# Kernel optimization log

Hardware: AMD Instinct MI355X
Metric: run time of the kernel (lower is better)

## Reference

```python
import jax, jax.numpy as jnp
import numpy as np


def _lstm_scan(x_proj, Wr, units):
    """x_proj: [T, B, 4U] precomputed x@Wk + b. Keras gate order: i, f, g(c), o.
    Returns (all_h [T,B,U], last_h [B,U])."""
    B = x_proj.shape[1]
    h0 = jnp.zeros((B, units), x_proj.dtype)
    c0 = jnp.zeros((B, units), x_proj.dtype)

    def step(carry, xt):
        h, c = carry
        z = xt + h @ Wr                      # [B, 4U]
        i, f, g, o = jnp.split(z, 4, axis=-1)
        i = jax.nn.sigmoid(i)
        f = jax.nn.sigmoid(f)
        g = jnp.tanh(g)
        o = jax.nn.sigmoid(o)
        c = f * c + i * g
        h = o * jnp.tanh(c)
        return (h, c), h

    (h_T, _), hs = jax.lax.scan(step, (h0, c0), x_proj)
    return hs, h_T


def bilstm(x, Wk_f, Wr_f, b_f, Wk_b, Wr_b, b_b):
    units = Wr_f.shape[0]
    # Precompute input projections for all timesteps (one big GEMM per direction)
    xp_f = (x @ Wk_f + b_f).transpose(1, 0, 2)             # [T, B, 4U]
    xp_b = (x[:, ::-1] @ Wk_b + b_b).transpose(1, 0, 2)    # reversed time

    fw_hs, fw_last = _lstm_scan(xp_f, Wr_f, units)         # [T,B,U], [B,U]
    bw_hs, bw_last = _lstm_scan(xp_b, Wr_b, units)

    fw_outputs = fw_hs.transpose(1, 0, 2)                  # [B, T, U]
    # go_backwards outputs are in reverse time order; K.reverse(_, 1) re-aligns
    bw_outputs = bw_hs.transpose(1, 0, 2)[:, ::-1]         # [B, T, U]

    outputs = jnp.concatenate([fw_outputs, bw_outputs], axis=-1)   # [B, T, 2U]
    last_output = jnp.concatenate([fw_last, bw_last], axis=-1)     # [B, 2U]
    return outputs, last_output


def setup_inputs() -> dict:
    key = jax.random.key(0)
    ks = jax.random.split(key, 6)
    B, T, D, U = 32, 512, 256, 256
    s_in = 1.0 / np.sqrt(D)
    s_rec = 1.0 / np.sqrt(U)
    return {
        "x": jax.random.normal(ks[0], (B, T, D), jnp.float32),
        "Wk_f": jax.random.normal(ks[1], (D, 4 * U), jnp.float32) * s_in,
        "Wr_f": jax.random.normal(ks[2], (U, 4 * U), jnp.float32) * s_rec,
        "b_f": jnp.zeros((4 * U,), jnp.float32),
        "Wk_b": jax.random.normal(ks[3], (D, 4 * U), jnp.float32) * s_in,
        "Wr_b": jax.random.normal(ks[4], (U, 4 * U), jnp.float32) * s_rec,
        "b_b": jnp.zeros((4 * U,), jnp.float32),
    }


def reference(x, Wk_f, Wr_f, b_f, Wk_b, Wr_b, b_b):
    return bilstm(x, Wk_f, Wr_f, b_f, Wk_b, Wr_b, b_b)
```

## Files before the change

### kernel.cpp

```cpp
#include <hip/hip_runtime.h>

#define T_STEPS 512
#define BATCH   32
#define DIM     256
#define UNITS   256
#define COLS4U  1024

typedef _Float16 half8  __attribute__((ext_vector_type(8)));
typedef _Float16 half4v __attribute__((ext_vector_type(4)));
typedef float    f32x4  __attribute__((ext_vector_type(4)));
typedef unsigned long long ull;
typedef ull      ull2   __attribute__((ext_vector_type(2)));

__device__ __forceinline__ float fsig(float x){ return 1.0f/(1.0f+__expf(-x)); }
__device__ __forceinline__ float ftanh(float x){
  float xx = fminf(fmaxf(x,-15.f),15.f);
  float e = __expf(2.f*xx);
  return (e-1.f)/(e+1.f);
}

__device__ __forceinline__ int swz(int b, int u){
  int g = u >> 3;
  int s = (g & 7) ^ (b & 7);
  return b*512 + (g>>3)*128 + s*16 + (u & 7)*2;
}

__global__ __launch_bounds__(256, 2) void xproj(
    const float* __restrict__ x,
    const float* __restrict__ Wk_f, const float* __restrict__ b_f,
    const float* __restrict__ Wk_b, const float* __restrict__ b_b,
    _Float16* __restrict__ xph)
{
  const int bx  = blockIdx.x;
  const int dir = bx >> 8;
  const int cg  = (bx >> 5) & 7;
  const int tg  = bx & 31;
  const int tid = threadIdx.x;
  const int w   = tid >> 6;
  const int lane= tid & 63;
  const int l15 = lane & 15;
  const int l4  = lane >> 4;

  const float* Wk = dir ? Wk_b : Wk_f;
  const float* bs = dir ? b_b  : b_f;

  const int col0 = cg*128 + w*32;

  half8 Bf[2][8];
  float bias[2];
#pragma unroll
  for (int nt=0; nt<2; nt++){
    const int col = col0 + nt*16 + l15;
    bias[nt] = bs[col];
#pragma unroll
    for (int kk=0; kk<8; kk++){
      half8 v;
#pragma unroll
      for (int r=0; r<8; r++) v[r] = (_Float16)Wk[(size_t)(kk*32 + l4*8 + r)*COLS4U + col];
      Bf[nt][kk] = v;
    }
  }

  for (int tt=0; tt<16; ++tt){
    const int t   = tg*16 + tt;
    const int tin = dir ? (T_STEPS-1-t) : t;

    half8 Af[2][8];
#pragma unroll
    for (int mt=0; mt<2; mt++){
      const int b = mt*16 + l15;
#pragma unroll
      for (int kk=0; kk<8; kk++){
        const float* xp_ = x + ((size_t)b*T_STEPS + tin)*DIM + kk*32 + l4*8;
        f32x4 u0 = *(const f32x4*)xp_;
        f32x4 u1 = *(const f32x4*)(xp_ + 4);
        half8 v;
        v[0]=(_Float16)u0[0]; v[1]=(_Float16)u0[1]; v[2]=(_Float16)u0[2]; v[3]=(_Float16)u0[3];
        v[4]=(_Float16)u1[0]; v[5]=(_Float16)u1[1]; v[6]=(_Float16)u1[2]; v[7]=(_Float16)u1[3];
        Af[mt][kk] = v;
      }
    }

    f32x4 acc[2][2];
#pragma unroll
    for (int nt=0; nt<2; nt++){
      f32x4 a; a[0]=bias[nt]; a[1]=bias[nt]; a[2]=bias[nt]; a[3]=bias[nt];
      acc[nt][0]=a; acc[nt][1]=a;
    }
#pragma unroll
    for (int kk=0; kk<8; kk++)
#pragma unroll
      for (int nt=0; nt<2; nt++)
#pragma unroll
        for (int mt=0; mt<2; mt++)
          acc[nt][mt] = __builtin_amdgcn_mfma_f32_16x16x32_f16(Af[mt][kk], Bf[nt][kk], acc[nt][mt], 0,0,0);

#pragma unroll
    for (int nt=0; nt<2; nt++){
      const int col = col0 + nt*16 + l15;
#pragma unroll
      for (int mt=0; mt<2; mt++){
        half4v o;
        o[0]=(_Float16)acc[nt][mt][0]; o[1]=(_Float16)acc[nt][mt][1];
        o[2]=(_Float16)acc[nt][mt][2]; o[3]=(_Float16)acc[nt][mt][3];
        *(ull*)(xph + ((size_t)(dir*T_STEPS + t)*COLS4U + col)*BATCH + mt*16 + l4*4)
            = __builtin_bit_cast(ull, o);
      }
    }
  }
}

__global__ __launch_bounds__(512, 2) void bilstm_scan4(
    const float* __restrict__ Wr_f, const float* __restrict__ Wr_b,
    float* __restrict__ out,
    const _Float16* __restrict__ xph,
    unsigned* __restrict__ slices)
{
  const int dir  = blockIdx.x >> 1;
  const int half = blockIdx.x & 1;
  const int tid  = threadIdx.x;
  const int w    = tid >> 6;
  const int lane = tid & 63;
  const int l15  = lane & 15;
  const int l4   = lane >> 4;

  const float* Wr = dir ? Wr_b : Wr_f;

  const int uloc   = w*16 + l15;
  const int unit   = half*128 + uloc;
  const int outcol = dir*256 + unit;

  __shared__ _Float16 hlds[2][BATCH*UNITS];

  half8 Bf[4][8];
#pragma unroll
  for (int q=0; q<4; q++){
    const int col = q*256 + unit;
#pragma unroll
    for (int kk=0; kk<8; kk++){
      half8 v;
#pragma unroll
      for (int r=0; r<8; r++) v[r] = (_Float16)Wr[(size_t)(kk*32 + l4*8 + r)*COLS4U + col];
      Bf[q][kk] = v;
      __builtin_amdgcn_sched_barrier(0);
    }
  }

  {
    half8 z;
#pragma unroll
    for (int e=0; e<8; e++) z[e] = (_Float16)0.f;
    for (int i=tid; i<BATCH*UNITS/8; i+=512) ((half8*)hlds[0])[i] = z;
  }
  __syncthreads();

  const int b_r = tid >> 4;
  const int c0  = (tid & 15) * 8;
  const int pbase = (1-half)*128;

  float cst[8];
#pragma unroll
  for (int i=0;i<8;i++) cst[i]=0.f;
  bool spin_ok = true;

  ull xpv[8];
#pragma unroll
  for (int q=0;q<4;q++)
#pragma unroll
    for (int mt=0;mt<2;mt++)
      xpv[q*2+mt] = *(const ull*)(xph + ((size_t)(dir*T_STEPS + 0)*COLS4U + q*256+unit)*BATCH + mt*16 + l4*4);

  for (int t=0; t<T_STEPS; ++t){
    f32x4 acc[2][4];
#pragma unroll
    for (int q=0;q<4;q++)
#pragma unroll
      for (int mt=0;mt<2;mt++){
        half4v hv = __builtin_bit_cast(half4v, xpv[q*2+mt]);
        f32x4 a; a[0]=(float)hv[0]; a[1]=(float)hv[1]; a[2]=(float)hv[2]; a[3]=(float)hv[3];
        acc[mt][q] = a;
      }

    const char* hpl = (const char*)hlds[t&1];
#pragma unroll
    for (int kk=0; kk<8; kk++){
      const int ul = kk*32 + l4*8;
      half8 a0 = *(const half8*)(hpl + swz(l15,    ul));
      half8 a1 = *(const half8*)(hpl + swz(16+l15, ul));
#pragma unroll
      for (int q=0;q<4;q++){
        acc[0][q] = __builtin_amdgcn_mfma_f32_16x16x32_f16(a0, Bf[q][kk], acc[0][q], 0,0,0);
        acc[1][q] = __builtin_amdgcn_mfma_f32_16x16x32_f16(a1, Bf[q][kk], acc[1][q], 0,0,0);
      }
    }

    const int tout = dir ? (T_STEPS-1-t) : t;
    const int par  = (t+1) & 1;
    unsigned* myslc = slices + ((size_t)(par*4 + dir*2 + half))*4096;
    const unsigned tgt_out = (unsigned)(t+1) & 0xFFFFu;
    char* hnx = (char*)hlds[(t+1)&1];
#pragma unroll
    for (int mt=0; mt<2; mt++){
#pragma unroll
      for (int r=0;r<4;r++){
        const int b = mt*16 + l4*4 + r;
        float iv = fsig (acc[mt][0][r]);
        float fv = fsig (acc[mt][1][r]);
        float gv = ftanh(acc[mt][2][r]);
        float ov = fsig (acc[mt][3][r]);
        float &c = cst[mt*4+r];
        c = fv*c + iv*gv;
        float hv = ov*ftanh(c);
        _Float16 hf = (_Float16)hv;
        if (t+1 < T_STEPS){
          unsigned word = ((unsigned)__builtin_bit_cast(unsigned short, hf) << 16) | tgt_out;
          __hip_atomic_store(&myslc[b*128 + uloc], word,
                             __ATOMIC_RELAXED, __HIP_MEMORY_SCOPE_AGENT);
        }
        *(_Float16*)(hnx + swz(b, unit)) = hf;
        out[((size_t)b*T_STEPS + tout)*(2*UNITS) + outcol] = hv;
        if (t == T_STEPS-1)
          out[(size_t)BATCH*T_STEPS*(2*UNITS) + (size_t)b*(2*UNITS) + outcol] = hv;
      }
    }

    if (t+1 < T_STEPS){
#pragma unroll
      for (int q=0;q<4;q++)
#pragma unroll
        for (int mt=0;mt<2;mt++)
          xpv[q*2+mt] = *(const ull*)(xph + ((size_t)(dir*T_STEPS + (t+1))*COLS4U + q*256+unit)*BATCH + mt*16 + l4*4);

      const ull* src = (const ull*)(slices + ((size_t)(par*4 + dir*2 + (1-half)))*4096
                                    + b_r*128 + c0);
      ull v0,v1,v2,v3;
      if (spin_ok){
        int sp = 0; bool ok;
        do {
          v0 = __hip_atomic_load(&src[0], __ATOMIC_RELAXED, __HIP_MEMORY_SCOPE_AGENT);
          v1 = __hip_atomic_load(&src[1], __ATOMIC_RELAXED, __HIP_MEMORY_SCOPE_AGENT);
          v2 = __hip_atomic_load(&src[2], __ATOMIC_RELAXED, __HIP_MEMORY_SCOPE_AGENT);
          v3 = __hip_atomic_load(&src[3], __ATOMIC_RELAXED, __HIP_MEMORY_SCOPE_AGENT);
          unsigned t0=(unsigned)v0, t1=(unsigned)(v0>>32), t2=(unsigned)v1, t3=(unsigned)(v1>>32);
          unsigned t4=(unsigned)v2, t5=(unsigned)(v2>>32), t6=(unsigned)v3, t7=(unsigned)(v3>>32);
          ok = ((t0&0xFFFF)==tgt_out) & ((t1&0xFFFF)==tgt_out) & ((t2&0xFFFF)==tgt_out)
             & ((t3&0xFFFF)==tgt_out) & ((t4&0xFFFF)==tgt_out) & ((t5&0xFFFF)==tgt_out)
             & ((t6&0xFFFF)==tgt_out) & ((t7&0xFFFF)==tgt_out);
          if (++sp > (1<<20)) { spin_ok = false; break; }
        } while(!ok);
      } else {
        v0 = __hip_atomic_load(&src[0], __ATOMIC_RELAXED, __HIP_MEMORY_SCOPE_AGENT);
        v1 = __hip_atomic_load(&src[1], __ATOMIC_RELAXED, __HIP_MEMORY_SCOPE_AGENT);
        v2 = __hip_atomic_load(&src[2], __ATOMIC_RELAXED, __HIP_MEMORY_SCOPE_AGENT);
        v3 = __hip_atomic_load(&src[3], __ATOMIC_RELAXED, __HIP_MEMORY_SCOPE_AGENT);
      }
      half8 hv;
      {
        unsigned wlo, whi;
        wlo=(unsigned)v0; whi=(unsigned)(v0>>32);
        hv[0]=__builtin_bit_cast(_Float16,(unsigned short)(wlo>>16));
        hv[1]=__builtin_bit_cast(_Float16,(unsigned short)(whi>>16));
        wlo=(unsigned)v1; whi=(unsigned)(v1>>32);
        hv[2]=__builtin_bit_cast(_Float16,(unsigned short)(wlo>>16));
        hv[3]=__builtin_bit_cast(_Float16,(unsigned short)(whi>>16));
        wlo=(unsigned)v2; whi=(unsigned)(v2>>32);
        hv[4]=__builtin_bit_cast(_Float16,(unsigned short)(wlo>>16));
        hv[5]=__builtin_bit_cast(_Float16,(unsigned short)(whi>>16));
        wlo=(unsigned)v3; whi=(unsigned)(v3>>32);
        hv[6]=__builtin_bit_cast(_Float16,(unsigned short)(wlo>>16));
        hv[7]=__builtin_bit_cast(_Float16,(unsigned short)(whi>>16));
      }
      *(half8*)(hnx + swz(b_r, pbase + c0)) = hv;
    }
    __syncthreads();
  }
}

__global__ __launch_bounds__(256,1) void bilstm_mfma(
    const float* __restrict__ x,
    const float* __restrict__ Wk_f, const float* __restrict__ Wr_f, const float* __restrict__ b_f,
    const float* __restrict__ Wk_b, const float* __restrict__ Wr_b, const float* __restrict__ b_b,
    float* __restrict__ out,
    unsigned short* __restrict__ slices,
    unsigned* __restrict__ flags)
{
  const int dir = blockIdx.x >> 2;
  const int g4  = blockIdx.x & 3;
  const int tid = threadIdx.x;
  const int w   = tid >> 6;
  const int lane= tid & 63;
  const int l15 = lane & 15;
  const int l4  = lane >> 4;

  const float* Wk = dir ? Wk_b : Wk_f;
  const float* Wr = dir ? Wr_b : Wr_f;
  const float* bs = dir ? b_b  : b_f;

  const int u0b   = g4*64;
  const int upl   = u0b + w*16 + l15;
  const int outcol= dir*256 + upl;

  __shared__ _Float16 xlds[BATCH*DIM];
  __shared__ _Float16 hlds[2][BATCH*UNITS];

  half8 Bf[4][16];
#pragma unroll
  for (int q=0;q<4;q++){
    const int col = q*256 + upl;
#pragma unroll
    for (int kk=0;kk<16;kk++){
      const float* Ws = (kk<8) ? Wk : Wr;
      const int k0 = (kk&7)*32 + l4*8;
      half8 v;
#pragma unroll
      for (int r=0;r<8;r++) v[r] = (_Float16)Ws[(size_t)(k0+r)*COLS4U + col];
      Bf[q][kk] = v;
      __builtin_amdgcn_sched_barrier(0);
    }
  }

  float bias[4];
#pragma unroll
  for (int q=0;q<4;q++) bias[q] = bs[q*256 + upl];

  {
    half8 z;
#pragma unroll
    for (int e=0;e<8;e++) z[e] = (_Float16)0.f;
    for (int i=tid; i<BATCH*UNITS/8; i+=256) ((half8*)hlds[0])[i] = z;
  }

  const int bx  = tid >> 3;
  const int d0x = (tid & 7) * 32;
  float xr[32];
  {
    const int tin0 = dir ? (T_STEPS-1) : 0;
    const float* xp = x + ((size_t)bx*T_STEPS + tin0)*DIM + d0x;
#pragma unroll
    for (int i=0;i<8;i++){
      f32x4 v = *(const f32x4*)(xp + i*4);
      xr[i*4+0]=v[0]; xr[i*4+1]=v[1]; xr[i*4+2]=v[2]; xr[i*4+3]=v[3];
    }
#pragma unroll
    for (int j=0;j<4;j++){
      half8 hh;
#pragma unroll
      for (int e=0;e<8;e++) hh[e] = (_Float16)xr[j*8+e];
      *(half8*)((char*)xlds + swz(bx, d0x + j*8)) = hh;
    }
  }
  __syncthreads();

  float cst[8];
#pragma unroll
  for (int i=0;i<8;i++) cst[i]=0.f;
  bool spin_ok = true;

  for (int t=0; t<T_STEPS; ++t){
    if (t+1 < T_STEPS){
      const int tin = dir ? (T_STEPS-2-t) : (t+1);
      const float* xp = x + ((size_t)bx*T_STEPS + tin)*DIM + d0x;
#pragma unroll
      for (int i=0;i<8;i++){
        f32x4 v = *(const f32x4*)(xp + i*4);
        xr[i*4+0]=v[0]; xr[i*4+1]=v[1]; xr[i*4+2]=v[2]; xr[i*4+3]=v[3];
      }
    }

    f32x4 acc[2][4];
#pragma unroll
    for (int q=0;q<4;q++){
      f32x4 a; a[0]=bias[q]; a[1]=bias[q]; a[2]=bias[q]; a[3]=bias[q];
      acc[0][q]=a; acc[1][q]=a;
    }
    const char* hpl = (const char*)hlds[t&1];
#pragma unroll
    for (int kk=0;kk<16;kk++){
      const char* pl = (kk<8) ? (const char*)xlds : hpl;
      const int ul = (kk&7)*32 + l4*8;
      half8 a0 = *(const half8*)(pl + swz(l15,      ul));
      half8 a1 = *(const half8*)(pl + swz(16+l15,   ul));
#pragma unroll
      for (int q=0;q<4;q++){
        acc[0][q] = __builtin_amdgcn_mfma_f32_16x16x32_f16(a0, Bf[q][kk], acc[0][q], 0,0,0);
        acc[1][q] = __builtin_amdgcn_mfma_f32_16x16x32_f16(a1, Bf[q][kk], acc[1][q], 0,0,0);
      }
    }

    const int tout = dir ? (T_STEPS-1-t) : t;
    unsigned short* slc = slices + (((size_t)((t+1)&1))*8 + dir*4 + g4)*2048;
    char* hnx = (char*)hlds[(t+1)&1];
#pragma unroll
    for (int mt=0; mt<2; mt++){
#pragma unroll
      for (int r=0;r<4;r++){
        const int b = mt*16 + l4*4 + r;
        float iv = fsig (acc[mt][0][r]);
        float fv = fsig (acc[mt][1][r]);
        float gv = ftanh(acc[mt][2][r]);
        float ov = fsig (acc[mt][3][r]);
        float &c = cst[mt*4+r];
        c = fv*c + iv*gv;
        float hval = ov*ftanh(c);
        out[((size_t)b*T_STEPS + tout)*(2*UNITS) + outcol] = hval;
        if (t == T_STEPS-1)
          out[(size_t)BATCH*T_STEPS*(2*UNITS) + (size_t)b*(2*UNITS) + outcol] = hval;
        _Float16 hf = (_Float16)hval;
        *(_Float16*)(hnx + swz(b, upl)) = hf;
        if (t+1 < T_STEPS)
          __hip_atomic_store(&slc[b*64 + (w*16+l15)],
                             __builtin_bit_cast(unsigned short, hf),
                             __ATOMIC_RELAXED, __HIP_MEMORY_SCOPE_AGENT);
      }
    }
    __syncthreads();

    if (t+1 < T_STEPS){
      if (tid == 192)
        __hip_atomic_store(&flags[(dir*4+g4)*32], (unsigned)(t+1),
                           __ATOMIC_RELAXED, __HIP_MEMORY_SCOPE_AGENT);
#pragma unroll
      for (int j=0;j<4;j++){
        half8 hh;
#pragma unroll
        for (int e=0;e<8;e++) hh[e] = (_Float16)xr[j*8+e];
        *(half8*)((char*)xlds + swz(bx, d0x + j*8)) = hh;
      }
      if (w < 3){
        const int p = w + (w >= g4);
        const unsigned target = (unsigned)(t+1);
        if (spin_ok){
          int sp = 0;
          while (__hip_atomic_load(&flags[(dir*4+p)*32],
                                   __ATOMIC_RELAXED, __HIP_MEMORY_SCOPE_AGENT) < target){
            if (++sp > (1<<22)) { spin_ok = false; break; }
          }
        }
        const ull* src = (const ull*)(slices + (((size_t)((t+1)&1))*8 + dir*4 + p)*2048);
        const int bsl = lane >> 1;
        const int u00 = (lane & 1) * 32;
#pragma unroll
        for (int j=0;j<4;j++){
          ull v0 = __hip_atomic_load(&src[lane*8 + 2*j  ], __ATOMIC_RELAXED, __HIP_MEMORY_SCOPE_AGENT);
          ull v1 = __hip_atomic_load(&src[lane*8 + 2*j+1], __ATOMIC_RELAXED, __HIP_MEMORY_SCOPE_AGENT);
          ull2 vv; vv[0]=v0; vv[1]=v1;
          *(ull2*)(hnx + swz(bsl, p*64 + u00 + j*8)) = vv;
        }
      }
      __syncthreads();
    }
  }
}

extern "C" void kernel_launch(void* const* d_in, const int* in_sizes, int n_in,
                              void* d_out, int out_size, void* d_ws, size_t ws_size,
                              hipStream_t stream) {
  const float* x    = (const float*)d_in[0];
  const float* Wk_f = (const float*)d_in[1];
  const float* Wr_f = (const float*)d_in[2];
  const float* b_f  = (const float*)d_in[3];
  const float* Wk_b = (const float*)d_in[4];
  const float* Wr_b = (const float*)d_in[5];
  const float* b_b  = (const float*)d_in[6];
  float* out = (float*)d_out;

  const size_t XPH = (size_t)2*T_STEPS*COLS4U*BATCH*sizeof(_Float16);
  const size_t SL  = (size_t)2*2*2*BATCH*128*sizeof(unsigned);

  if (ws_size >= XPH + SL) {
    _Float16* xph    = (_Float16*)d_ws;
    unsigned* slices = (unsigned*)((char*)d_ws + XPH);
    xproj<<<512, 256, 0, stream>>>(x, Wk_f, b_f, Wk_b, b_b, xph);
    bilstm_scan4<<<4, 512, 0, stream>>>(Wr_f, Wr_b, out, xph, slices);
  } else {
    unsigned short* slices = (unsigned short*)d_ws;
    unsigned* flags = (unsigned*)((char*)d_ws + 65536);
    hipMemsetAsync((char*)d_ws + 65536, 0, 1024, stream);
    bilstm_mfma<<<8, 256, 0, stream>>>(x, Wk_f, Wr_f, b_f, Wk_b, Wr_b, b_b,
                                       out, slices, flags);
  }
}
```

Measured before the change: 2.842 ms.

## Split LSTM scan across 8 blocks placed on shared XCDs via runtime election

Replaces the 4-block (2 per direction, 512 threads) recurrent scan with 8 blocks of 256 threads, 4 per direction, each owning 64 units. The kernel launches 64 candidate blocks, which record their XCC_ID in a registration table and then elect blocks that share an XCD. When placement succeeds, h exchange uses volatile stores and loads instead of agent-scope atomics, on the expectation that same-XCD L2 coherence makes plain accesses visible. This halves per-block MFMA work per step but requires every step to gather slices from three peers instead of one, and its correctness rests on the co-location assumption and on spin timeouts.

Result: slower. 6.429 ms (+126.2%).

```diff
diff --git a/kernel.cpp b/kernel.cpp
--- a/kernel.cpp
+++ b/kernel.cpp
@@ -5,6 +5,7 @@
 #define DIM     256
 #define UNITS   256
 #define COLS4U  1024
+#define NCAND   64
 
 typedef _Float16 half8  __attribute__((ext_vector_type(8)));
 typedef _Float16 half4v __attribute__((ext_vector_type(4)));
@@ -14,15 +15,13 @@
 
 __device__ __forceinline__ float fsig(float x){ return 1.0f/(1.0f+__expf(-x)); }
 __device__ __forceinline__ float ftanh(float x){
-  float xx = fminf(fmaxf(x,-15.f),15.f);
-  float e = __expf(2.f*xx);
+  float xx=fminf(fmaxf(x,-15.f),15.f);
+  float e=__expf(2.f*xx);
   return (e-1.f)/(e+1.f);
 }
-
-__device__ __forceinline__ int swz(int b, int u){
-  int g = u >> 3;
-  int s = (g & 7) ^ (b & 7);
-  return b*512 + (g>>3)*128 + s*16 + (u & 7)*2;
+__device__ __forceinline__ int swz(int b,int u){
+  int g=u>>3; int s=(g&7)^(b&7);
+  return b*512 + (g>>3)*128 + s*16 + (u&7)*2;
 }
 
 __global__ __launch_bounds__(256, 2) void xproj(
@@ -110,38 +109,26 @@
   }
 }
 
-__global__ __launch_bounds__(512, 2) void bilstm_scan4(
-    const float* __restrict__ Wr_f, const float* __restrict__ Wr_b,
-    float* __restrict__ out,
-    const _Float16* __restrict__ xph,
-    unsigned* __restrict__ slices)
+template<int MODE>
+__device__ __forceinline__ void scan_body(
+    int dir, int g4, const float* __restrict__ Wr, float* __restrict__ out,
+    const _Float16* __restrict__ xph, unsigned* __restrict__ slices,
+    _Float16 (*hlds)[BATCH*UNITS])
 {
-  const int dir  = blockIdx.x >> 1;
-  const int half = blockIdx.x & 1;
-  const int tid  = threadIdx.x;
-  const int w    = tid >> 6;
-  const int lane = tid & 63;
-  const int l15  = lane & 15;
-  const int l4   = lane >> 4;
-
-  const float* Wr = dir ? Wr_b : Wr_f;
-
-  const int uloc   = w*16 + l15;
-  const int unit   = half*128 + uloc;
-  const int outcol = dir*256 + unit;
-
-  __shared__ _Float16 hlds[2][BATCH*UNITS];
+  const int tid=threadIdx.x;
+  const int w=tid>>6, lane=tid&63, l15=lane&15, l4=lane>>4;
+  const int uloc=w*16+l15, unit=g4*64+uloc, outcol=dir*256+unit;
 
   half8 Bf[4][8];
 #pragma unroll
-  for (int q=0; q<4; q++){
-    const int col = q*256 + unit;
-#pragma unroll
-    for (int kk=0; kk<8; kk++){
+  for(int q=0;q<4;q++){
+    const int col=q*256+unit;
+#pragma unroll
+    for(int kk=0;kk<8;kk++){
       half8 v;
 #pragma unroll
-      for (int r=0; r<8; r++) v[r] = (_Float16)Wr[(size_t)(kk*32 + l4*8 + r)*COLS4U + col];
-      Bf[q][kk] = v;
+      for(int r=0;r<8;r++) v[r]=(_Float16)Wr[(size_t)(kk*32+l4*8+r)*COLS4U+col];
+      Bf[q][kk]=v;
       __builtin_amdgcn_sched_barrier(0);
     }
   }
@@ -149,131 +136,176 @@
   {
     half8 z;
 #pragma unroll
-    for (int e=0; e<8; e++) z[e] = (_Float16)0.f;
-    for (int i=tid; i<BATCH*UNITS/8; i+=512) ((half8*)hlds[0])[i] = z;
+    for(int e=0;e<8;e++) z[e]=(_Float16)0.f;
+    for(int i=tid;i<BATCH*UNITS/8;i+=256) ((half8*)hlds[0])[i]=z;
   }
   __syncthreads();
 
-  const int b_r = tid >> 4;
-  const int c0  = (tid & 15) * 8;
-  const int pbase = (1-half)*128;
-
   float cst[8];
 #pragma unroll
-  for (int i=0;i<8;i++) cst[i]=0.f;
-  bool spin_ok = true;
+  for(int i=0;i<8;i++) cst[i]=0.f;
+  bool spin_ok=true;
 
   ull xpv[8];
 #pragma unroll
-  for (int q=0;q<4;q++)
-#pragma unroll
-    for (int mt=0;mt<2;mt++)
-      xpv[q*2+mt] = *(const ull*)(xph + ((size_t)(dir*T_STEPS + 0)*COLS4U + q*256+unit)*BATCH + mt*16 + l4*4);
-
-  for (int t=0; t<T_STEPS; ++t){
+  for(int q=0;q<4;q++)
+#pragma unroll
+    for(int mt=0;mt<2;mt++)
+      xpv[q*2+mt]=*(const ull*)(xph+((size_t)(dir*T_STEPS+0)*COLS4U+q*256+unit)*BATCH+mt*16+l4*4);
+
+  const int b_r=lane>>1, u0r=(lane&1)*32;
+  const int pw=(w<3)?(w+(w>=g4)):0;
+
+  for(int t=0;t<T_STEPS;++t){
     f32x4 acc[2][4];
 #pragma unroll
-    for (int q=0;q<4;q++)
-#pragma unroll
-      for (int mt=0;mt<2;mt++){
-        half4v hv = __builtin_bit_cast(half4v, xpv[q*2+mt]);
-        f32x4 a; a[0]=(float)hv[0]; a[1]=(float)hv[1]; a[2]=(float)hv[2]; a[3]=(float)hv[3];
-        acc[mt][q] = a;
-      }
-
-    const char* hpl = (const char*)hlds[t&1];
-#pragma unroll
-    for (int kk=0; kk<8; kk++){
-      const int ul = kk*32 + l4*8;
-      half8 a0 = *(const half8*)(hpl + swz(l15,    ul));
-      half8 a1 = *(const half8*)(hpl + swz(16+l15, ul));
-#pragma unroll
-      for (int q=0;q<4;q++){
-        acc[0][q] = __builtin_amdgcn_mfma_f32_16x16x32_f16(a0, Bf[q][kk], acc[0][q], 0,0,0);
-        acc[1][q] = __builtin_amdgcn_mfma_f32_16x16x32_f16(a1, Bf[q][kk], acc[1][q], 0,0,0);
-      }
-    }
-
-    const int tout = dir ? (T_STEPS-1-t) : t;
-    const int par  = (t+1) & 1;
-    unsigned* myslc = slices + ((size_t)(par*4 + dir*2 + half))*4096;
-    const unsigned tgt_out = (unsigned)(t+1) & 0xFFFFu;
-    char* hnx = (char*)hlds[(t+1)&1];
-#pragma unroll
-    for (int mt=0; mt<2; mt++){
-#pragma unroll
-      for (int r=0;r<4;r++){
-        const int b = mt*16 + l4*4 + r;
-        float iv = fsig (acc[mt][0][r]);
-        float fv = fsig (acc[mt][1][r]);
-        float gv = ftanh(acc[mt][2][r]);
-        float ov = fsig (acc[mt][3][r]);
-        float &c = cst[mt*4+r];
-        c = fv*c + iv*gv;
-        float hv = ov*ftanh(c);
-        _Float16 hf = (_Float16)hv;
-        if (t+1 < T_STEPS){
-          unsigned word = ((unsigned)__builtin_bit_cast(unsigned short, hf) << 16) | tgt_out;
-          __hip_atomic_store(&myslc[b*128 + uloc], word,
-                             __ATOMIC_RELAXED, __HIP_MEMORY_SCOPE_AGENT);
+    for(int q=0;q<4;q++)
+#pragma unroll
+      for(int mt=0;mt<2;mt++){
+        half4v hv=__builtin_bit_cast(half4v,xpv[q*2+mt]);
+        f32x4 a; a[0]=(float)hv[0];a[1]=(float)hv[1];a[2]=(float)hv[2];a[3]=(float)hv[3];
+        acc[mt][q]=a;
+      }
+
+    const char* hpl=(const char*)hlds[t&1];
+#pragma unroll
+    for(int kk=0;kk<8;kk++){
+      const int ul=kk*32+l4*8;
+      half8 a0=*(const half8*)(hpl+swz(l15,ul));
+      half8 a1=*(const half8*)(hpl+swz(16+l15,ul));
+#pragma unroll
+      for(int q=0;q<4;q++){
+        acc[0][q]=__builtin_amdgcn_mfma_f32_16x16x32_f16(a0,Bf[q][kk],acc[0][q],0,0,0);
+        acc[1][q]=__builtin_amdgcn_mfma_f32_16x16x32_f16(a1,Bf[q][kk],acc[1][q],0,0,0);
+      }
+    }
+
+    const int tout=dir?(T_STEPS-1-t):t;
+    const int par=(t+1)&1;
+    unsigned* myslc=slices+((size_t)(par*8+dir*4+g4))*2048;
+    const unsigned tgt=(unsigned)(t+1)&0xFFFFu;
+    char* hnx=(char*)hlds[(t+1)&1];
+#pragma unroll
+    for(int mt=0;mt<2;mt++){
+#pragma unroll
+      for(int r=0;r<4;r++){
+        const int b=mt*16+l4*4+r;
+        float iv=fsig(acc[mt][0][r]);
+        float fv=fsig(acc[mt][1][r]);
+        float gv=ftanh(acc[mt][2][r]);
+        float ov=fsig(acc[mt][3][r]);
+        float &c=cst[mt*4+r];
+        c=fv*c+iv*gv;
+        float hv=ov*ftanh(c);
+        _Float16 hf=(_Float16)hv;
+        if(t+1<T_STEPS){
+          unsigned word=((unsigned)__builtin_bit_cast(unsigned short,hf)<<16)|tgt;
+          if(MODE==0) *(volatile unsigned*)&myslc[b*64+uloc]=word;
+          else __hip_atomic_store(&myslc[b*64+uloc],word,__ATOMIC_RELAXED,__HIP_MEMORY_SCOPE_AGENT);
         }
-        *(_Float16*)(hnx + swz(b, unit)) = hf;
-        out[((size_t)b*T_STEPS + tout)*(2*UNITS) + outcol] = hv;
-        if (t == T_STEPS-1)
-          out[(size_t)BATCH*T_STEPS*(2*UNITS) + (size_t)b*(2*UNITS) + outcol] = hv;
-      }
-    }
-
-    if (t+1 < T_STEPS){
-#pragma unroll
-      for (int q=0;q<4;q++)
-#pragma unroll
-        for (int mt=0;mt<2;mt++)
-          xpv[q*2+mt] = *(const ull*)(xph + ((size_t)(dir*T_STEPS + (t+1))*COLS4U + q*256+unit)*BATCH + mt*16 + l4*4);
-
-      const ull* src = (const ull*)(slices + ((size_t)(par*4 + dir*2 + (1-half)))*4096
-                                    + b_r*128 + c0);
-      ull v0,v1,v2,v3;
-      if (spin_ok){
-        int sp = 0; bool ok;
-        do {
-          v0 = __hip_atomic_load(&src[0], __ATOMIC_RELAXED, __HIP_MEMORY_SCOPE_AGENT);
-          v1 = __hip_atomic_load(&src[1], __ATOMIC_RELAXED, __HIP_MEMORY_SCOPE_AGENT);
-          v2 = __hip_atomic_load(&src[2], __ATOMIC_RELAXED, __HIP_MEMORY_SCOPE_AGENT);
-          v3 = __hip_atomic_load(&src[3], __ATOMIC_RELAXED, __HIP_MEMORY_SCOPE_AGENT);
-          unsigned t0=(unsigned)v0, t1=(unsigned)(v0>>32), t2=(unsigned)v1, t3=(unsigned)(v1>>32);
-          unsigned t4=(unsigned)v2, t5=(unsigned)(v2>>32), t6=(unsigned)v3, t7=(unsigned)(v3>>32);
-          ok = ((t0&0xFFFF)==tgt_out) & ((t1&0xFFFF)==tgt_out) & ((t2&0xFFFF)==tgt_out)
-             & ((t3&0xFFFF)==tgt_out) & ((t4&0xFFFF)==tgt_out) & ((t5&0xFFFF)==tgt_out)
-             & ((t6&0xFFFF)==tgt_out) & ((t7&0xFFFF)==tgt_out);
-          if (++sp > (1<<20)) { spin_ok = false; break; }
-        } while(!ok);
-      } else {
-        v0 = __hip_atomic_load(&src[0], __ATOMIC_RELAXED, __HIP_MEMORY_SCOPE_AGENT);
-        v1 = __hip_atomic_load(&src[1], __ATOMIC_RELAXED, __HIP_MEMORY_SCOPE_AGENT);
-        v2 = __hip_atomic_load(&src[2], __ATOMIC_RELAXED, __HIP_MEMORY_SCOPE_AGENT);
-        v3 = __hip_atomic_load(&src[3], __ATOMIC_RELAXED, __HIP_MEMORY_SCOPE_AGENT);
-      }
-      half8 hv;
-      {
-        unsigned wlo, whi;
-        wlo=(unsigned)v0; whi=(unsigned)(v0>>32);
-        hv[0]=__builtin_bit_cast(_Float16,(unsigned short)(wlo>>16));
-        hv[1]=__builtin_bit_cast(_Float16,(unsigned short)(whi>>16));
-        wlo=(unsigned)v1; whi=(unsigned)(v1>>32);
-        hv[2]=__builtin_bit_cast(_Float16,(unsigned short)(wlo>>16));
-        hv[3]=__builtin_bit_cast(_Float16,(unsigned short)(whi>>16));
-        wlo=(unsigned)v2; whi=(unsigned)(v2>>32);
-        hv[4]=__builtin_bit_cast(_Float16,(unsigned short)(wlo>>16));
-        hv[5]=__builtin_bit_cast(_Float16,(unsigned short)(whi>>16));
-        wlo=(unsigned)v3; whi=(unsigned)(v3>>32);
-        hv[6]=__builtin_bit_cast(_Float16,(unsigned short)(wlo>>16));
-        hv[7]=__builtin_bit_cast(_Float16,(unsigned short)(whi>>16));
-      }
-      *(half8*)(hnx + swz(b_r, pbase + c0)) = hv;
+        *(_Float16*)(hnx+swz(b,unit))=hf;
+        out[((size_t)b*T_STEPS+tout)*(2*UNITS)+outcol]=hv;
+        if(t==T_STEPS-1)
+          out[(size_t)BATCH*T_STEPS*(2*UNITS)+(size_t)b*(2*UNITS)+outcol]=hv;
+      }
+    }
+
+    if(t+1<T_STEPS){
+#pragma unroll
+      for(int q=0;q<4;q++)
+#pragma unroll
+        for(int mt=0;mt<2;mt++)
+          xpv[q*2+mt]=*(const ull*)(xph+((size_t)(dir*T_STEPS+(t+1))*COLS4U+q*256+unit)*BATCH+mt*16+l4*4);
+
+      if(w<3){
+        const unsigned* src=slices+((size_t)(par*8+dir*4+pw))*2048 + b_r*64 + u0r;
+        unsigned wbuf[32];
+        if(spin_ok){
+          int sp=0; bool ok;
+          do{
+            ok=true;
+#pragma unroll
+            for(int k=0;k<32;k++){
+              unsigned v=(MODE==0)? *(volatile const unsigned*)(src+k)
+                 : __hip_atomic_load(src+k,__ATOMIC_RELAXED,__HIP_MEMORY_SCOPE_AGENT);
+              wbuf[k]=v; ok &= ((v&0xFFFFu)==tgt);
+            }
+            if(++sp>(1<<17)){spin_ok=false;break;}
+          }while(!ok);
+        } else {
+#pragma unroll
+          for(int k=0;k<32;k++)
+            wbuf[k]=(MODE==0)? *(volatile const unsigned*)(src+k)
+               : __hip_atomic_load(src+k,__ATOMIC_RELAXED,__HIP_MEMORY_SCOPE_AGENT);
+        }
+#pragma unroll
+        for(int j=0;j<4;j++){
+          half8 hh;
+#pragma unroll
+          for(int e=0;e<8;e++)
+            hh[e]=__builtin_bit_cast(_Float16,(unsigned short)(wbuf[j*8+e]>>16));
+          *(half8*)(hnx+swz(b_r,pw*64+u0r+j*8))=hh;
+        }
+      }
     }
     __syncthreads();
   }
+}
+
+__global__ __launch_bounds__(256,1) void bilstm_scan_xcd(
+    const float* __restrict__ Wr_f, const float* __restrict__ Wr_b,
+    float* __restrict__ out, const _Float16* __restrict__ xph,
+    unsigned* __restrict__ slices, unsigned* __restrict__ regtab)
+{
+  __shared__ _Float16 hlds[2][BATCH*UNITS];
+  __shared__ unsigned stab[NCAND];
+  __shared__ int sinfo[2];
+  const int tid=threadIdx.x;
+
+  if(tid==0){
+    unsigned xv;
+    asm volatile("s_getreg_b32 %0, hwreg(HW_REG_XCC_ID)":"=s"(xv));
+    __hip_atomic_store(&regtab[blockIdx.x],0x100u|(xv&0xFu),
+                       __ATOMIC_RELAXED,__HIP_MEMORY_SCOPE_AGENT);
+  }
+  if(tid<NCAND){
+    unsigned v; int sp=0;
+    for(;;){
+      v=__hip_atomic_load(&regtab[tid],__ATOMIC_RELAXED,__HIP_MEMORY_SCOPE_AGENT);
+      if(__all((v&0x100u)!=0)) break;
+      if(++sp>(1<<17)) break;
+    }
+    stab[tid]=v;
+  }
+  __syncthreads();
+
+  if(tid==0){
+    bool full=true;
+    for(int i=0;i<NCAND;i++) if(!(stab[i]&0x100u)){full=false;break;}
+    int role=-1, mode=0;
+    if(full){
+      int cnt[8]={0,0,0,0,0,0,0,0};
+      for(int i=0;i<NCAND;i++) cnt[stab[i]&7]++;
+      int x0=-1,x1=-1;
+      for(int a=0;a<8;a++) if(cnt[a]>=4){x0=a;break;}
+      for(int a=0;a<8;a++) if(a!=x0&&cnt[a]>=4){x1=a;break;}
+      if(x1<0) x1=x0;
+      const int myb=(int)blockIdx.x;
+      const int myx=stab[myb]&7;
+      int rank=0;
+      for(int i=0;i<myb;i++) if((stab[i]&7)==myx) rank++;
+      if(x1==x0){ if(myx==x0&&rank<8) role=rank; }
+      else{ if(myx==x0&&rank<4) role=rank; else if(myx==x1&&rank<4) role=4+rank; }
+    } else { mode=1; if(blockIdx.x<8) role=(int)blockIdx.x; }
+    sinfo[0]=role; sinfo[1]=mode;
+  }
+  __syncthreads();
+  const int role=sinfo[0];
+  if(role<0) return;
+  const int dir=role>>2, g4=role&3;
+  const float* Wr=dir?Wr_b:Wr_f;
+  if(sinfo[1]==0) scan_body<0>(dir,g4,Wr,out,xph,slices,hlds);
+  else            scan_body<1>(dir,g4,Wr,out,xph,slices,hlds);
 }
 
 __global__ __launch_bounds__(256,1) void bilstm_mfma(
@@ -465,13 +497,16 @@
   float* out = (float*)d_out;
 
   const size_t XPH = (size_t)2*T_STEPS*COLS4U*BATCH*sizeof(_Float16);
-  const size_t SL  = (size_t)2*2*2*BATCH*128*sizeof(unsigned);
-
-  if (ws_size >= XPH + SL) {
+  const size_t SL  = (size_t)2*8*2048*sizeof(unsigned);
+  const size_t RT  = 256;
+
+  if (ws_size >= XPH + SL + RT) {
     _Float16* xph    = (_Float16*)d_ws;
     unsigned* slices = (unsigned*)((char*)d_ws + XPH);
+    unsigned* regtab = (unsigned*)((char*)d_ws + XPH + SL);
+    hipMemsetAsync(regtab, 0, RT, stream);
     xproj<<<512, 256, 0, stream>>>(x, Wk_f, b_f, Wk_b, b_b, xph);
-    bilstm_scan4<<<4, 512, 0, stream>>>(Wr_f, Wr_b, out, xph, slices);
+    bilstm_scan_xcd<<<NCAND, 256, 0, stream>>>(Wr_f, Wr_b, out, xph, slices, regtab);
   } else {
     unsigned short* slices = (unsigned short*)d_ws;
     unsigned* flags = (unsigned*)((char*)d_ws + 65536);
```

## Co-locate scan blocks on one XCC and exchange hidden state via L2-coherent loads

Applied to the files above, without the earlier changes.

The scan kernel now launches 64 candidate blocks that each report their XCC id. Block 0 then picks four blocks sharing an XCC to run the four direction/half roles, and the remaining blocks exit. The hidden-state exchange between the two halves uses sc0 global loads and stores (intended to stay coherent within one XCC's L2), with a fallback to the agent-scope atomic path after a spin timeout. This aims to cut cross-XCC communication latency per timestep, at the cost of an extra memset, a registration handshake, dual stores, and reliance on all candidate blocks being co-resident.

Measured after the change: 9.428 ms. +231.7%, slower.

```diff
diff --git a/kernel.cpp b/kernel.cpp
--- a/kernel.cpp
+++ b/kernel.cpp
@@ -5,24 +5,35 @@
 #define DIM     256
 #define UNITS   256
 #define COLS4U  1024
+#define NCAND   64
 
 typedef _Float16 half8  __attribute__((ext_vector_type(8)));
 typedef _Float16 half4v __attribute__((ext_vector_type(4)));
 typedef float    f32x4  __attribute__((ext_vector_type(4)));
+typedef unsigned uint4v __attribute__((ext_vector_type(4)));
 typedef unsigned long long ull;
 typedef ull      ull2   __attribute__((ext_vector_type(2)));
 
 __device__ __forceinline__ float fsig(float x){ return 1.0f/(1.0f+__expf(-x)); }
 __device__ __forceinline__ float ftanh(float x){
-  float xx = fminf(fmaxf(x,-15.f),15.f);
-  float e = __expf(2.f*xx);
+  float xx=fminf(fmaxf(x,-15.f),15.f);
+  float e=__expf(2.f*xx);
   return (e-1.f)/(e+1.f);
 }
-
-__device__ __forceinline__ int swz(int b, int u){
-  int g = u >> 3;
-  int s = (g & 7) ^ (b & 7);
-  return b*512 + (g>>3)*128 + s*16 + (u & 7)*2;
+__device__ __forceinline__ int swz(int b,int u){
+  int g=u>>3; int s=(g&7)^(b&7);
+  return b*512 + (g>>3)*128 + s*16 + (u&7)*2;
+}
+
+__device__ __forceinline__ void ld8_sc0(const unsigned* p, uint4v& a, uint4v& b){
+  asm volatile(
+    "global_load_dwordx4 %0, %2, off sc0\n\t"
+    "global_load_dwordx4 %1, %2, off offset:16 sc0\n\t"
+    "s_waitcnt vmcnt(0)"
+    : "=&v"(a), "=&v"(b) : "v"(p) : "memory");
+}
+__device__ __forceinline__ void st1_sc0(unsigned* p, unsigned v){
+  asm volatile("global_store_dword %0, %1, off sc0" :: "v"(p), "v"(v) : "memory");
 }
 
 __global__ __launch_bounds__(256, 2) void xproj(
@@ -110,27 +121,22 @@
   }
 }
 
-__global__ __launch_bounds__(512, 2) void bilstm_scan4(
-    const float* __restrict__ Wr_f, const float* __restrict__ Wr_b,
-    float* __restrict__ out,
+__device__ __forceinline__ void scan_body(
+    int dir, int half_, bool fast0,
+    const float* __restrict__ Wr, float* __restrict__ out,
     const _Float16* __restrict__ xph,
-    unsigned* __restrict__ slices)
+    unsigned* __restrict__ fastslc, unsigned* __restrict__ safeslc,
+    _Float16 (*hlds)[BATCH*UNITS])
 {
-  const int dir  = blockIdx.x >> 1;
-  const int half = blockIdx.x & 1;
   const int tid  = threadIdx.x;
   const int w    = tid >> 6;
   const int lane = tid & 63;
   const int l15  = lane & 15;
   const int l4   = lane >> 4;
 
-  const float* Wr = dir ? Wr_b : Wr_f;
-
   const int uloc   = w*16 + l15;
-  const int unit   = half*128 + uloc;
+  const int unit   = half_*128 + uloc;
   const int outcol = dir*256 + unit;
-
-  __shared__ _Float16 hlds[2][BATCH*UNITS];
 
   half8 Bf[4][8];
 #pragma unroll
@@ -156,12 +162,13 @@
 
   const int b_r = tid >> 4;
   const int c0  = (tid & 15) * 8;
-  const int pbase = (1-half)*128;
+  const int pbase = (1-half_)*128;
 
   float cst[8];
 #pragma unroll
   for (int i=0;i<8;i++) cst[i]=0.f;
-  bool spin_ok = true;
+  bool use_fast = fast0;
+  bool safe_ok  = true;
 
   ull xpv[8];
 #pragma unroll
@@ -196,8 +203,8 @@
 
     const int tout = dir ? (T_STEPS-1-t) : t;
     const int par  = (t+1) & 1;
-    unsigned* myslc = slices + ((size_t)(par*4 + dir*2 + half))*4096;
-    const unsigned tgt_out = (unsigned)(t+1) & 0xFFFFu;
+    const size_t wslot = ((size_t)(par*4 + dir*2 + half_))*4096;
+    const unsigned tgt = (unsigned)(t+1) & 0xFFFFu;
     char* hnx = (char*)hlds[(t+1)&1];
 #pragma unroll
     for (int mt=0; mt<2; mt++){
@@ -213,8 +220,9 @@
         float hv = ov*ftanh(c);
         _Float16 hf = (_Float16)hv;
         if (t+1 < T_STEPS){
-          unsigned word = ((unsigned)__builtin_bit_cast(unsigned short, hf) << 16) | tgt_out;
-          __hip_atomic_store(&myslc[b*128 + uloc], word,
+          unsigned word = ((unsigned)__builtin_bit_cast(unsigned short, hf) << 16) | tgt;
+          st1_sc0(&fastslc[wslot + b*128 + uloc], word);
+          __hip_atomic_store(&safeslc[wslot + b*128 + uloc], word,
                              __ATOMIC_RELAXED, __HIP_MEMORY_SCOPE_AGENT);
         }
         *(_Float16*)(hnx + swz(b, unit)) = hf;
@@ -231,49 +239,127 @@
         for (int mt=0;mt<2;mt++)
           xpv[q*2+mt] = *(const ull*)(xph + ((size_t)(dir*T_STEPS + (t+1))*COLS4U + q*256+unit)*BATCH + mt*16 + l4*4);
 
-      const ull* src = (const ull*)(slices + ((size_t)(par*4 + dir*2 + (1-half)))*4096
-                                    + b_r*128 + c0);
-      ull v0,v1,v2,v3;
-      if (spin_ok){
-        int sp = 0; bool ok;
-        do {
-          v0 = __hip_atomic_load(&src[0], __ATOMIC_RELAXED, __HIP_MEMORY_SCOPE_AGENT);
-          v1 = __hip_atomic_load(&src[1], __ATOMIC_RELAXED, __HIP_MEMORY_SCOPE_AGENT);
-          v2 = __hip_atomic_load(&src[2], __ATOMIC_RELAXED, __HIP_MEMORY_SCOPE_AGENT);
-          v3 = __hip_atomic_load(&src[3], __ATOMIC_RELAXED, __HIP_MEMORY_SCOPE_AGENT);
-          unsigned t0=(unsigned)v0, t1=(unsigned)(v0>>32), t2=(unsigned)v1, t3=(unsigned)(v1>>32);
-          unsigned t4=(unsigned)v2, t5=(unsigned)(v2>>32), t6=(unsigned)v3, t7=(unsigned)(v3>>32);
-          ok = ((t0&0xFFFF)==tgt_out) & ((t1&0xFFFF)==tgt_out) & ((t2&0xFFFF)==tgt_out)
-             & ((t3&0xFFFF)==tgt_out) & ((t4&0xFFFF)==tgt_out) & ((t5&0xFFFF)==tgt_out)
-             & ((t6&0xFFFF)==tgt_out) & ((t7&0xFFFF)==tgt_out);
-          if (++sp > (1<<20)) { spin_ok = false; break; }
-        } while(!ok);
+      const size_t rslot = ((size_t)(par*4 + dir*2 + (1-half_)))*4096;
+      const unsigned* fsrc = fastslc + rslot + b_r*128 + c0;
+      const unsigned* ssrc = safeslc + rslot + b_r*128 + c0;
+      unsigned wv[8];
+      bool got = false;
+
+      if (use_fast){
+        int sp = 0;
+        for(;;){
+          uint4v a, b2;
+          ld8_sc0(fsrc, a, b2);
+          wv[0]=a[0]; wv[1]=a[1]; wv[2]=a[2]; wv[3]=a[3];
+          wv[4]=b2[0]; wv[5]=b2[1]; wv[6]=b2[2]; wv[7]=b2[3];
+          bool ok = true;
+#pragma unroll
+          for (int k=0;k<8;k++) ok &= ((wv[k]&0xFFFFu)==tgt);
+          if (ok){ got = true; break; }
+          if (++sp > 4096){ use_fast = false; break; }
+        }
+      }
+      if (!got){
+        if (safe_ok){
+          int sp = 0;
+          for(;;){
+            bool ok = true;
+#pragma unroll
+            for (int k=0;k<8;k++){
+              wv[k] = __hip_atomic_load(ssrc+k, __ATOMIC_RELAXED, __HIP_MEMORY_SCOPE_AGENT);
+              ok &= ((wv[k]&0xFFFFu)==tgt);
+            }
+            if (ok) break;
+            if (++sp > (1<<20)){ safe_ok = false; break; }
+          }
+        } else {
+#pragma unroll
+          for (int k=0;k<8;k++)
+            wv[k] = __hip_atomic_load(ssrc+k, __ATOMIC_RELAXED, __HIP_MEMORY_SCOPE_AGENT);
+        }
+      }
+
+      half8 hh;
+#pragma unroll
+      for (int e=0;e<8;e++)
+        hh[e] = __builtin_bit_cast(_Float16,(unsigned short)(wv[e]>>16));
+      *(half8*)(hnx + swz(b_r, pbase + c0)) = hh;
+    }
+    __syncthreads();
+  }
+}
+
+__global__ __launch_bounds__(512,1) void bilstm_scan_pair(
+    const float* __restrict__ Wr_f, const float* __restrict__ Wr_b,
+    float* __restrict__ out, const _Float16* __restrict__ xph,
+    unsigned* __restrict__ fastslc, unsigned* __restrict__ safeslc,
+    unsigned* __restrict__ regtab)
+{
+  __shared__ _Float16 hlds[2][BATCH*UNITS];
+  __shared__ unsigned stab[NCAND];
+  __shared__ int sinfo[2];
+  const int tid = threadIdx.x;
+  const int bid = (int)blockIdx.x;
+
+  if (tid==0){
+    unsigned xv;
+    asm volatile("s_getreg_b32 %0, hwreg(HW_REG_XCC_ID)":"=s"(xv));
+    __hip_atomic_store(&regtab[bid], 0x100u|(xv&0xFu),
+                       __ATOMIC_RELAXED,__HIP_MEMORY_SCOPE_AGENT);
+  }
+
+  if (bid==0){
+    if (tid<NCAND){
+      unsigned v; int sp=0;
+      for(;;){
+        v=__hip_atomic_load(&regtab[tid],__ATOMIC_RELAXED,__HIP_MEMORY_SCOPE_AGENT);
+        if (__all((v&0x100u)!=0u)) break;
+        if (++sp>(1<<18)) break;
+      }
+      stab[tid]=v;
+    }
+    __syncthreads();
+    if (tid==0){
+      bool full=true;
+      for (int i=0;i<NCAND;i++) if(!(stab[i]&0x100u)){full=false;break;}
+      unsigned dec;
+      int xs=-1;
+      if (full){
+        int cnt[16];
+        for (int a=0;a<16;a++) cnt[a]=0;
+        for (int i=0;i<NCAND;i++) cnt[stab[i]&0xF]++;
+        for (int a=0;a<16;a++) if (cnt[a]>=4){xs=a;break;}
+      }
+      if (xs>=0){
+        unsigned ids[4]; int n=0;
+        for (int i=0;i<NCAND && n<4;i++) if ((int)(stab[i]&0xF)==xs) ids[n++]=(unsigned)i;
+        dec = 0x80000000u | (ids[0]) | (ids[1]<<6) | (ids[2]<<12) | (ids[3]<<18);
       } else {
-        v0 = __hip_atomic_load(&src[0], __ATOMIC_RELAXED, __HIP_MEMORY_SCOPE_AGENT);
-        v1 = __hip_atomic_load(&src[1], __ATOMIC_RELAXED, __HIP_MEMORY_SCOPE_AGENT);
-        v2 = __hip_atomic_load(&src[2], __ATOMIC_RELAXED, __HIP_MEMORY_SCOPE_AGENT);
-        v3 = __hip_atomic_load(&src[3], __ATOMIC_RELAXED, __HIP_MEMORY_SCOPE_AGENT);
-      }
-      half8 hv;
-      {
-        unsigned wlo, whi;
-        wlo=(unsigned)v0; whi=(unsigned)(v0>>32);
-        hv[0]=__builtin_bit_cast(_Float16,(unsigned short)(wlo>>16));
-        hv[1]=__builtin_bit_cast(_Float16,(unsigned short)(whi>>16));
-        wlo=(unsigned)v1; whi=(unsigned)(v1>>32);
-        hv[2]=__builtin_bit_cast(_Float16,(unsigned short)(wlo>>16));
-        hv[3]=__builtin_bit_cast(_Float16,(unsigned short)(whi>>16));
-        wlo=(unsigned)v2; whi=(unsigned)(v2>>32);
-        hv[4]=__builtin_bit_cast(_Float16,(unsigned short)(wlo>>16));
-        hv[5]=__builtin_bit_cast(_Float16,(unsigned short)(whi>>16));
-        wlo=(unsigned)v3; whi=(unsigned)(v3>>32);
-        hv[6]=__builtin_bit_cast(_Float16,(unsigned short)(wlo>>16));
-        hv[7]=__builtin_bit_cast(_Float16,(unsigned short)(whi>>16));
-      }
-      *(half8*)(hnx + swz(b_r, pbase + c0)) = hv;
-    }
-    __syncthreads();
-  }
+        dec = 0x80000000u | (1u<<30) | 0u | (1u<<6) | (2u<<12) | (3u<<18);
+      }
+      __hip_atomic_store(&regtab[NCAND], dec, __ATOMIC_RELAXED,__HIP_MEMORY_SCOPE_AGENT);
+    }
+  }
+
+  if (tid==0){
+    unsigned dec=0; int sp=0;
+    for(;;){
+      dec=__hip_atomic_load(&regtab[NCAND],__ATOMIC_RELAXED,__HIP_MEMORY_SCOPE_AGENT);
+      if (dec & 0x80000000u) break;
+      if (++sp>(1<<22)){ dec = 0x80000000u|(1u<<30)|0u|(1u<<6)|(2u<<12)|(3u<<18); break; }
+    }
+    int role=-1;
+    const int mode = (int)((dec>>30)&1u);
+#pragma unroll
+    for (int i=0;i<4;i++) if (((dec>>(6*i))&63u)==(unsigned)bid) role=i;
+    sinfo[0]=role; sinfo[1]=mode;
+  }
+  __syncthreads();
+  const int role=sinfo[0];
+  if (role<0) return;
+  const int dir=role>>1, hf=role&1;
+  const float* Wr = dir ? Wr_b : Wr_f;
+  scan_body(dir, hf, sinfo[1]==0, Wr, out, xph, fastslc, safeslc, hlds);
 }
 
 __global__ __launch_bounds__(256,1) void bilstm_mfma(
@@ -464,14 +550,19 @@
   const float* b_b  = (const float*)d_in[6];
   float* out = (float*)d_out;
 
-  const size_t XPH = (size_t)2*T_STEPS*COLS4U*BATCH*sizeof(_Float16);
-  const size_t SL  = (size_t)2*2*2*BATCH*128*sizeof(unsigned);
-
-  if (ws_size >= XPH + SL) {
-    _Float16* xph    = (_Float16*)d_ws;
-    unsigned* slices = (unsigned*)((char*)d_ws + XPH);
+  const size_t XPH  = (size_t)2*T_STEPS*COLS4U*BATCH*sizeof(_Float16);
+  const size_t SL   = (size_t)8*4096*sizeof(unsigned);
+  const size_t RT   = 512;
+
+  if (ws_size >= XPH + 2*SL + RT) {
+    _Float16* xph     = (_Float16*)d_ws;
+    unsigned* fastslc = (unsigned*)((char*)d_ws + XPH);
+    unsigned* safeslc = (unsigned*)((char*)d_ws + XPH + SL);
+    unsigned* regtab  = (unsigned*)((char*)d_ws + XPH + 2*SL);
+    hipMemsetAsync((char*)d_ws + XPH, 0, 2*SL + RT, stream);
     xproj<<<512, 256, 0, stream>>>(x, Wk_f, b_f, Wk_b, b_b, xph);
-    bilstm_scan4<<<4, 512, 0, stream>>>(Wr_f, Wr_b, out, xph, slices);
+    bilstm_scan_pair<<<NCAND, 512, 0, stream>>>(Wr_f, Wr_b, out, xph,
+                                                fastslc, safeslc, regtab);
   } else {
     unsigned short* slices = (unsigned short*)d_ws;
     unsigned* flags = (unsigned*)((char*)d_ws + 65536);
```
